# Performance work log

Hardware: AMD Instinct MI355X
Metric: run time of the kernel (lower is better)

## Reference

```python
import jax, jax.numpy as jnp
import numpy as np

# db1 (Haar) filters, replicating the torch module's pywt-derived constants.
_s = np.float32(1.0 / np.sqrt(2.0))
_dl = np.array([_s, _s], np.float32)    # dec_lo[::-1]
_dh = np.array([_s, -_s], np.float32)   # dec_hi[::-1]
_rl = np.array([_s, _s], np.float32)    # rec_lo
_rh = np.array([_s, -_s], np.float32)   # rec_hi
# filters[k][i,j] = a[j]*b[i]  (torch: a.unsqueeze(0)*b.unsqueeze(1)) == outer(b, a)
DEC = jnp.asarray(np.stack([np.outer(_dl, _dl) / 2.0, np.outer(_dh, _dl), np.outer(_dl, _dh), np.outer(_dh, _dh)], 0))  # [4,2,2]
REC = jnp.asarray(np.stack([np.outer(_rl, _rl) * 2.0, np.outer(_rh, _rl), np.outer(_rl, _rh), np.outer(_rh, _rh)], 0))  # [4,2,2]


def wt(x):
    # stride-2 2x2 conv per channel == linear mix of 2x2 blocks; fused over all channels
    B, C, H, W = x.shape
    xb = x.reshape(B, C, H // 2, 2, W // 2, 2)
    y = jnp.einsum('kpq,bchpwq->bckhw', DEC, xb)  # [B,C,4,H/2,W/2]
    y = jnp.concatenate([y[:, :, :1], (y[:, :, 1:] + 1.0) * 0.5], axis=2)  # rescale HF bands
    return y.reshape(B, 4 * C, H // 2, W // 2)


def iwt(y):
    B, C4, H, W = y.shape
    C = C4 // 4
    yb = y.reshape(B, C, 4, H, W)
    yb = jnp.concatenate([yb[:, :, :1], 2.0 * yb[:, :, 1:] - 1.0], axis=2)  # undo HF rescale
    x = jnp.einsum('kpq,bckhw->bchpwq', REC, yb)  # conv_transpose2d, stride 2, no overlap
    return x.reshape(B, C, 2 * H, 2 * W)


def conv3x3(x, w, b):
    y = jax.lax.conv_general_dilated(x, w, (1, 1), ((1, 1), (1, 1)), dimension_numbers=('NCHW', 'OIHW', 'NCHW'))
    return y + b[None, :, None, None]


def setup_inputs() -> dict:
    key = jax.random.key(0)
    ks = jax.random.split(key, 20)
    B, Cin, H, W = 8, 1, 512, 512
    c = 16
    inp = {'x': jax.random.normal(ks[0], (B, Cin, H, W), jnp.float32)}
    specs = [('conv1', c, 4 * Cin), ('conv2', 4 * c, 4 * c), ('conv3', 16 * c, 16 * c), ('conv4', 64 * c, 64 * c),
             ('convd1', 4, c), ('convd2', c, 2 * c), ('convd3', 4 * c, 8 * c), ('convd4', 16 * c, 32 * c)]
    for idx, (name, o, i) in enumerate(specs):
        kw, kb = jax.random.split(ks[1 + idx])
        inp[name + '_w'] = jax.random.normal(kw, (o, i, 3, 3), jnp.float32) / np.float32(np.sqrt(i * 9))
        inp[name + '_b'] = jax.random.normal(kb, (o,), jnp.float32) * 0.01
    return inp


def reference(x, conv1_w, conv1_b, conv2_w, conv2_b, conv3_w, conv3_b, conv4_w, conv4_b,
              convd1_w, convd1_b, convd2_w, convd2_b, convd3_w, convd3_b, convd4_w, convd4_b):
    lrelu = lambda t: jax.nn.leaky_relu(t, 0.2)
    w1 = wt(x);  c1 = lrelu(conv3x3(w1, conv1_w, conv1_b))
    w2 = wt(c1); c2 = lrelu(conv3x3(w2, conv2_w, conv2_b))
    w3 = wt(c2); c3 = lrelu(conv3x3(w3, conv3_w, conv3_b))
    w4 = wt(c3); c4 = lrelu(conv3x3(w4, conv4_w, conv4_b))
    c5 = lrelu(conv3x3(c4, conv4_w, conv4_b))  # conv4 reused, as in the torch module
    c6 = conv3x3(c5, conv4_w, conv4_b)
    ic4 = lrelu(c6 + w4)
    ic3 = lrelu(conv3x3(jnp.concatenate([c3, iwt(ic4)], 1), convd4_w, convd4_b))
    ic2 = lrelu(conv3x3(jnp.concatenate([c2, iwt(ic3)], 1), convd3_w, convd3_b))
    ic1 = lrelu(conv3x3(jnp.concatenate([c1, iwt(ic2)], 1), convd2_w, convd2_b))
    iw1 = lrelu(conv3x3(ic1, convd1_w, convd1_b))
    logits = iwt(iw1)
    return jax.nn.sigmoid(logits)
```

## Files before the change

kernel.cpp:

```cpp
#include <hip/hip_runtime.h>
#include <cstddef>


typedef unsigned short u16;
typedef unsigned int u32;
typedef __bf16 bf16x8 __attribute__((ext_vector_type(8)));
typedef float floatx4 __attribute__((ext_vector_type(4)));
typedef u16 u16x4 __attribute__((ext_vector_type(4)));
typedef u16 u16x8 __attribute__((ext_vector_type(8)));

__device__ __forceinline__ float b2f(u16 h) {
    union { u32 u; float f; } x; x.u = ((u32)h) << 16; return x.f;
}
__device__ __forceinline__ u16 f2b(float f) {
    union { float f; u32 u; } x; x.f = f;
    return (u16)((x.u + 0x7FFFu + ((x.u >> 16) & 1u)) >> 16);
}
__device__ __forceinline__ float lrelu_f(float v) { return v > 0.f ? v : 0.2f * v; }

__device__ __forceinline__ void gld16(const u16* g, u16* l) {
    __builtin_amdgcn_global_load_lds(
        (const __attribute__((address_space(1))) u32*)(const void*)g,
        (__attribute__((address_space(3))) u32*)(void*)l, 16, 0, 0);
}

template<int NT>
__global__ __launch_bounds__(256)
void conv_mfma_k(const u16* __restrict__ in, int Cin, int iWp, int iImg,
                 const u16* __restrict__ wb, const float* __restrict__ bias,
                 const u16* __restrict__ skip, int sC, int sWp, int sImg, int spad,
                 u16* __restrict__ out, int Cst, int oWp, int oImg, int opad,
                 int logW, int logH)
{
    constexpr int BM = 128, BN = NT * 32;
    constexpr int ASZ = BM * 32;
    constexpr int BSZ = BN * 32;
    __shared__ u16 At[2 * ASZ];
    __shared__ u16 Bt[2 * BSZ];

    const int tid = threadIdx.x;
    const int wid = tid >> 6, lane = tid & 63;
    const int W = 1 << logW, H = 1 << logH;
    const int mBase = blockIdx.x * BM;
    const int nBase = blockIdx.y * BN;
    const int K = 9 * Cin;
    const int kg = lane & 3;
    const int rr = lane >> 2;
    const int kgs = kg ^ ((rr >> 1) & 3);

    const u16 *gA0, *gA1, *gB0, *gB1 = nullptr;
    {
        int m0 = mBase + wid * 32 + rr;
        int px0 = m0 & (W - 1), py0 = (m0 >> logW) & (H - 1), pb0 = m0 >> (logW + logH);
        gA0 = in + ((size_t)pb0 * iImg + (size_t)py0 * iWp + px0) * Cin + kgs * 8;
        int m1 = m0 + 16;
        int px1 = m1 & (W - 1), py1 = (m1 >> logW) & (H - 1), pb1 = m1 >> (logW + logH);
        gA1 = in + ((size_t)pb1 * iImg + (size_t)py1 * iWp + px1) * Cin + kgs * 8;
    }
    if constexpr (NT == 4) {
        gB0 = wb + (size_t)(nBase + wid * 32 + rr) * K + kgs * 8;
        gB1 = wb + (size_t)(nBase + wid * 32 + 16 + rr) * K + kgs * 8;
    } else {
        gB0 = wb + (size_t)(nBase + wid * 16 + rr) * K + kgs * 8;
    }
    u16* lA0 = &At[wid * 1024];
    u16* lA1 = &At[wid * 1024 + 512];
    u16* lB0 = (NT == 4) ? &Bt[wid * 1024] : &Bt[wid * 512];
    u16* lB1 = (NT == 4) ? &Bt[wid * 1024 + 512] : nullptr;

    const int wm = wid >> 1, wn = wid & 1;
    const int fm = lane & 15;
    const int fk = ((lane >> 4) * 8) ^ (((fm >> 1) & 3) << 3);

    floatx4 acc[4][NT] = {};

    const int nChunks = K / 32;
    const size_t rowStep = (size_t)(iWp - 2) * Cin;
    int cbn = 0, tap = 0;

    auto stage = [&](int buf) {
        gld16(gA0, lA0 + buf * ASZ);
        gld16(gA1, lA1 + buf * ASZ);
        gld16(gB0, lB0 + buf * BSZ);
        if constexpr (NT == 4) gld16(gB1, lB1 + buf * BSZ);
        size_t dA = 32;
        cbn += 32;
        if (cbn == Cin) { cbn = 0; ++tap; dA = ((tap % 3 == 0) ? rowStep : (size_t)Cin) - (size_t)(Cin - 32); }
        gA0 += dA; gA1 += dA;
        gB0 += 32;
        if constexpr (NT == 4) gB1 += 32;
    };

    auto compute = [&](int buf) {
        const u16* Ab = &At[buf * ASZ];
        const u16* Bb = &Bt[buf * BSZ];
        bf16x8 af[4], bfr[NT];
#pragma unroll
        for (int mt = 0; mt < 4; ++mt)
            af[mt] = *(const bf16x8*)&Ab[(wm * 64 + mt * 16 + fm) * 32 + fk];
#pragma unroll
        for (int nt = 0; nt < NT; ++nt)
            bfr[nt] = *(const bf16x8*)&Bb[(wn * (NT * 16) + nt * 16 + fm) * 32 + fk];
        __builtin_amdgcn_s_setprio(1);
#pragma unroll
        for (int mt = 0; mt < 4; ++mt)
#pragma unroll
            for (int nt = 0; nt < NT; ++nt)
                acc[mt][nt] = __builtin_amdgcn_mfma_f32_16x16x32_bf16(af[mt], bfr[nt], acc[mt][nt], 0, 0, 0);
        __builtin_amdgcn_s_setprio(0);
    };

    stage(0);
    __syncthreads();
    for (int kc = 0; kc < nChunks; kc += 2) {
        stage(1);
        compute(0);
        __syncthreads();
        if (kc + 2 < nChunks) stage(0);
        compute(1);
        __syncthreads();
    }

    const int rq = (lane >> 4) * 4;
#pragma unroll
    for (int mt = 0; mt < 4; ++mt) {
        const int mrow = mBase + wm * 64 + mt * 16 + rq;
#pragma unroll
        for (int r = 0; r < 4; ++r) {
            int m2 = mrow + r;
            int px = m2 & (W - 1), py = (m2 >> logW) & (H - 1), pb = m2 >> (logW + logH);
            size_t ob = ((size_t)pb * oImg + (size_t)(py + opad) * oWp + (px + opad)) * Cst;
            size_t sb = 0;
            if (skip) sb = ((size_t)pb * sImg + (size_t)(py + spad) * sWp + (px + spad)) * sC;
#pragma unroll
            for (int nt = 0; nt < NT; ++nt) {
                int n = nBase + wn * (NT * 16) + nt * 16 + fm;
                float v = acc[mt][nt][r] + bias[n];
                if (skip) v += b2f(skip[sb + n]);
                v = lrelu_f(v);
                out[ob + n] = f2b(v);
            }
        }
    }
}

__global__ __launch_bounds__(256)
void conv_n16_k(const u16* __restrict__ in, int iWp, int iImg,
                const u16* __restrict__ wb, const float* __restrict__ bias,
                u16* __restrict__ out, int logW, int logH)
{
    __shared__ u16 At[128 * 32];
    __shared__ u16 Bt[16 * 32];
    const int tid = threadIdx.x;
    const int wid = tid >> 6, lane = tid & 63;
    const int W = 1 << logW, H = 1 << logH;
    const int mBase = blockIdx.x * 128;
    const int kg = lane & 3, rr = lane >> 2;
    const int kgs = kg ^ ((rr >> 1) & 3);

    const u16 *gA0, *gA1;
    {
        int m0 = mBase + wid * 32 + rr;
        int px0 = m0 & (W - 1), py0 = (m0 >> logW) & (H - 1), pb0 = m0 >> (logW + logH);
        gA0 = in + ((size_t)pb0 * iImg + (size_t)py0 * iWp + px0) * 32 + kgs * 8;
        int m1 = m0 + 16;
        int px1 = m1 & (W - 1), py1 = (m1 >> logW) & (H - 1), pb1 = m1 >> (logW + logH);
        gA1 = in + ((size_t)pb1 * iImg + (size_t)py1 * iWp + px1) * 32 + kgs * 8;
    }
    const u16* gB = wb + (size_t)rr * 288 + kgs * 8;
    u16* lA0 = &At[wid * 1024];
    u16* lA1 = &At[wid * 1024 + 512];

    const int fm = lane & 15;
    const int fk = ((lane >> 4) * 8) ^ (((fm >> 1) & 3) << 3);
    floatx4 acc[2] = {};
    const size_t rowStep = (size_t)(iWp - 2) * 32;

    for (int tap = 0; tap < 9; ++tap) {
        gld16(gA0, lA0);
        gld16(gA1, lA1);
        if (wid == 0) gld16(gB, &Bt[0]);
        __syncthreads();
        bf16x8 bf = *(const bf16x8*)&Bt[fm * 32 + fk];
#pragma unroll
        for (int mt = 0; mt < 2; ++mt) {
            bf16x8 af = *(const bf16x8*)&At[(wid * 32 + mt * 16 + fm) * 32 + fk];
            acc[mt] = __builtin_amdgcn_mfma_f32_16x16x32_bf16(af, bf, acc[mt], 0, 0, 0);
        }
        __syncthreads();
        size_t dA = (tap % 3 == 2) ? rowStep : (size_t)32;
        gA0 += dA; gA1 += dA; gB += 32;
    }

    const int rq = (lane >> 4) * 4;
    const float bn = bias[fm];
#pragma unroll
    for (int mt = 0; mt < 2; ++mt) {
#pragma unroll
        for (int r = 0; r < 4; ++r) {
            int m2 = mBase + wid * 32 + mt * 16 + rq + r;
            out[(size_t)m2 * 16 + fm] = f2b(lrelu_f(acc[mt][r] + bn));
        }
    }
}

template<int CIN, int COUT>
__global__ __launch_bounds__(256)
void conv_direct_k(const u16* __restrict__ in, int Sin,
                   const float* __restrict__ w, const float* __restrict__ bias,
                   u16* __restrict__ out, int Sout, int oWp, int oImg, int opad,
                   int logW, int logH, int total)
{
    int m = blockIdx.x * 256 + threadIdx.x;
    if (m >= total) return;
    const int W = 1 << logW, H = 1 << logH;
    const int px = m & (W - 1);
    const int py = (m >> logW) & (H - 1);
    const int pb = m >> (logW + logH);
    float acc[COUT];
#pragma unroll
    for (int o = 0; o < COUT; ++o) acc[o] = bias[o];
    for (int tap = 0; tap < 9; ++tap) {
        int dy = tap / 3 - 1, dx = tap % 3 - 1;
        int iy = py + dy, ix = px + dx;
        if ((unsigned)iy >= (unsigned)H || (unsigned)ix >= (unsigned)W) continue;
        const u16* p = in + (size_t)((((pb << logH) + iy) << logW) + ix) * Sin;
        if constexpr (CIN == 4) {
            u16x4 v = *(const u16x4*)p;
#pragma unroll
            for (int ci = 0; ci < 4; ++ci) {
                float f = b2f(v[ci]);
#pragma unroll
                for (int o = 0; o < COUT; ++o) acc[o] += f * w[(o * CIN + ci) * 9 + tap];
            }
        } else {
#pragma unroll
            for (int c8 = 0; c8 < CIN / 8; ++c8) {
                u16x8 v = *(const u16x8*)(p + c8 * 8);
#pragma unroll
                for (int j = 0; j < 8; ++j) {
                    int ci = c8 * 8 + j;
                    float f = b2f(v[j]);
#pragma unroll
                    for (int o = 0; o < COUT; ++o) acc[o] += f * w[(o * CIN + ci) * 9 + tap];
                }
            }
        }
    }
    size_t ob = ((size_t)pb * oImg + (size_t)(py + opad) * oWp + (px + opad)) * Sout;
#pragma unroll
    for (int o = 0; o < COUT; ++o)
        out[ob + o] = f2b(lrelu_f(acc[o]));
}

__global__ __launch_bounds__(256)
void wt_in_k(const float* __restrict__ x, u16* __restrict__ out, int total)
{
    int idx = blockIdx.x * 256 + threadIdx.x;
    if (idx >= total) return;
    int wq = idx & 255, t = idx >> 8;
    int hq = t & 255, b = t >> 8;
    const float* p = x + ((size_t)b * 512 + 2 * hq) * 512 + 2 * wq;
    float a = p[0], bv = p[1], cv = p[512], d = p[513];
    u16x4 o = { f2b(0.25f * (a + bv + cv + d)),
                f2b(0.25f * (a + bv - cv - d) + 0.5f),
                f2b(0.25f * (a - bv + cv - d) + 0.5f),
                f2b(0.25f * (a - bv - cv + d) + 0.5f) };
    *(u16x4*)&out[(size_t)idx * 4] = o;
}

__global__ __launch_bounds__(256)
void wt_k(const u16* __restrict__ in, int Sin, int iWp, int iImg, int ipad,
          u16* __restrict__ out, int Sout, int oWp, int oImg, int opad,
          int logC, int logWo, int logHo, int total)
{
    int idx = blockIdx.x * 256 + threadIdx.x;
    if (idx >= total) return;
    const int C = 1 << logC, Wo = 1 << logWo, Ho = 1 << logHo;
    int c = idx & (C - 1); int t = idx >> logC;
    int wq = t & (Wo - 1); t >>= logWo;
    int hq = t & (Ho - 1); int b = t >> logHo;
    size_t p00 = ((size_t)b * iImg + (size_t)(2 * hq + ipad) * iWp + (2 * wq + ipad)) * Sin + c;
    float a  = b2f(in[p00]);
    float bv = b2f(in[p00 + Sin]);
    float cv = b2f(in[p00 + (size_t)iWp * Sin]);
    float d  = b2f(in[p00 + (size_t)iWp * Sin + Sin]);
    u16x4 o = { f2b(0.25f * (a + bv + cv + d)),
                f2b(0.25f * (a + bv - cv - d) + 0.5f),
                f2b(0.25f * (a - bv + cv - d) + 0.5f),
                f2b(0.25f * (a - bv - cv + d) + 0.5f) };
    *(u16x4*)&out[((size_t)b * oImg + (size_t)(hq + opad) * oWp + (wq + opad)) * Sout + 4 * c] = o;
}

__global__ __launch_bounds__(256)
void iwt_k(const u16* __restrict__ in, int Sin, int logC, int logW, int logH,
           u16* __restrict__ out, int Sout, int oWp, int oImg, int opad, int total)
{
    int idx = blockIdx.x * 256 + threadIdx.x;
    if (idx >= total) return;
    const int C = 1 << logC, W = 1 << logW;
    int c = idx & (C - 1); int t = idx >> logC;
    int wq = t & (W - 1); t >>= logW;
    int hq = t & ((1 << logH) - 1); int b = t >> logH;
    u16x4 v = *(const u16x4*)&in[(size_t)((((b << logH) + hq) << logW) + wq) * Sin + 4 * c];
    float y0 = b2f(v[0]);
    float y1 = 2.f * b2f(v[1]) - 1.f;
    float y2 = 2.f * b2f(v[2]) - 1.f;
    float y3 = 2.f * b2f(v[3]) - 1.f;
    float x00 = y0 + 0.5f * ( y1 + y2 + y3);
    float x01 = y0 + 0.5f * ( y1 - y2 - y3);
    float x10 = y0 + 0.5f * (-y1 + y2 - y3);
    float x11 = y0 + 0.5f * (-y1 - y2 + y3);
    size_t q = ((size_t)b * oImg + (size_t)(2 * hq + opad) * oWp + (2 * wq + opad)) * Sout + c;
    out[q] = f2b(x00);
    out[q + Sout] = f2b(x01);
    out[q + (size_t)oWp * Sout] = f2b(x10);
    out[q + (size_t)oWp * Sout + Sout] = f2b(x11);
}

__global__ __launch_bounds__(256)
void iwt_out_k(const u16* __restrict__ in, float* __restrict__ out, int total)
{
    int idx = blockIdx.x * 256 + threadIdx.x;
    if (idx >= total) return;
    int wq = idx & 255, t = idx >> 8;
    int hq = t & 255, b = t >> 8;
    u16x4 v = *(const u16x4*)&in[(size_t)idx * 4];
    float y0 = b2f(v[0]);
    float y1 = 2.f * b2f(v[1]) - 1.f;
    float y2 = 2.f * b2f(v[2]) - 1.f;
    float y3 = 2.f * b2f(v[3]) - 1.f;
    float x00 = y0 + 0.5f * ( y1 + y2 + y3);
    float x01 = y0 + 0.5f * ( y1 - y2 - y3);
    float x10 = y0 + 0.5f * (-y1 + y2 - y3);
    float x11 = y0 + 0.5f * (-y1 - y2 + y3);
    float* q = out + ((size_t)b * 512 + 2 * hq) * 512 + 2 * wq;
    q[0]   = 1.f / (1.f + __expf(-x00));
    q[1]   = 1.f / (1.f + __expf(-x01));
    q[512] = 1.f / (1.f + __expf(-x10));
    q[513] = 1.f / (1.f + __expf(-x11));
}

__global__ __launch_bounds__(256)
void prep_w_k(const float* __restrict__ src, u16* __restrict__ dst, int logCIN, int total)
{
    int idx = blockIdx.x * 256 + threadIdx.x;
    if (idx >= total) return;
    const int CIN = 1 << logCIN;
    int ci = idx & (CIN - 1);
    int q = idx >> logCIN;
    int tap = q % 9, o = q / 9;
    dst[idx] = f2b(src[((size_t)(o * CIN + ci)) * 9 + tap]);
}

__global__ __launch_bounds__(256)
void zb_k(u16* __restrict__ buf, int Wp, int Hp, int C, int total)
{
    int idx = blockIdx.x * 256 + threadIdx.x;
    if (idx >= total) return;
    int c8 = idx % (C / 8); int t = idx / (C / 8);
    int nbp = 2 * Wp + 2 * (Hp - 2);
    int p = t % nbp; int b = t / nbp;
    int y, x;
    if (p < Wp) { y = 0; x = p; }
    else if (p < 2 * Wp) { y = Hp - 1; x = p - Wp; }
    else { int q = p - 2 * Wp; y = 1 + (q >> 1); x = (q & 1) ? Wp - 1 : 0; }
    u16x8 z = {0, 0, 0, 0, 0, 0, 0, 0};
    *(u16x8*)&buf[((size_t)b * Hp * Wp + (size_t)y * Wp + x) * C + c8 * 8] = z;
}

extern "C" void kernel_launch(void* const* d_in, const int* in_sizes, int n_in,
                              void* d_out, int out_size, void* d_ws, size_t ws_size,
                              hipStream_t stream)
{
    const float* x   = (const float*)d_in[0];
    const float* c1w = (const float*)d_in[1];  const float* c1b = (const float*)d_in[2];
    const float* c2w = (const float*)d_in[3];  const float* c2b = (const float*)d_in[4];
    const float* c3w = (const float*)d_in[5];  const float* c3b = (const float*)d_in[6];
    const float* c4w = (const float*)d_in[7];  const float* c4b = (const float*)d_in[8];
    const float* d1w = (const float*)d_in[9];  const float* d1b = (const float*)d_in[10];
    const float* d2w = (const float*)d_in[11]; const float* d2b = (const float*)d_in[12];
    const float* d3w = (const float*)d_in[13]; const float* d3b = (const float*)d_in[14];
    const float* d4w = (const float*)d_in[15]; const float* d4b = (const float*)d_in[16];

    const size_t MiB = 1u << 20;
    char* base = (char*)d_ws;
    u16* c4wb = (u16*)base;
    u16* c3wb = c4wb + 9437184;
    u16* d4wb = c3wb + 589824;
    u16* d3wb = d4wb + 1179648;
    u16* c2wb = d3wb + 73728;
    u16* d2wb = c2wb + 36864;
    u16* CAT1p = (u16*)(base + 22  * MiB);
    u16* CAT2p = (u16*)(base + 55  * MiB);
    u16* CAT3p = (u16*)(base + 88  * MiB);
    u16* P1    = (u16*)(base + 123 * MiB);
    u16* P2    = (u16*)(base + 142 * MiB);
    u16* P3    = (u16*)(base + 161 * MiB);
    float* outp = (float*)d_out;

    u16* W2p = P1; u16* W4p = P1; u16* IC2 = P1;
    u16* W3p = P2; u16* C4p = P2; u16* IC4 = P2; u16* IC1 = P2;
    u16* W1  = P3; u16* C5p = P3; u16* IC3 = P3; u16* IW1 = P3;

    auto cdiv = [](int a, int b) { return (a + b - 1) / b; };
    auto prep = [&](const float* s, u16* d, int logCIN, int total) {
        prep_w_k<<<cdiv(total, 256), 256, 0, stream>>>(s, d, logCIN, total);
    };
    auto zb = [&](u16* buf, int Wp, int Hp, int C) {
        int total = 8 * (2 * Wp + 2 * (Hp - 2)) * (C / 8);
        zb_k<<<cdiv(total, 256), 256, 0, stream>>>(buf, Wp, Hp, C, total);
    };
    auto mfma = [&](const u16* in, int Cin, int iWp, int iImg,
                    const u16* w, const float* bi,
                    const u16* skip, int sC, int sWp, int sImg, int spad,
                    int Cout, u16* out, int Cst, int oWp, int oImg, int opad,
                    int logW, int logH) {
        int M = 8 << (logW + logH);
        if (Cout % 128 == 0) {
            dim3 g(M / 128, Cout / 128);
            conv_mfma_k<4><<<g, 256, 0, stream>>>(in, Cin, iWp, iImg, w, bi,
                                                  skip, sC, sWp, sImg, spad,
                                                  out, Cst, oWp, oImg, opad, logW, logH);
        } else {
            dim3 g(M / 128, Cout / 64);
            conv_mfma_k<2><<<g, 256, 0, stream>>>(in, Cin, iWp, iImg, w, bi,
                                                  skip, sC, sWp, sImg, spad,
                                                  out, Cst, oWp, oImg, opad, logW, logH);
        }
    };

    prep(c4w, c4wb, 10, 9437184);
    prep(c3w, c3wb, 8, 589824);
    prep(d4w, d4wb, 9, 1179648);
    prep(d3w, d3wb, 7, 73728);
    prep(c2w, c2wb, 6, 36864);
    prep(d2w, d2wb, 5, 4608);
    zb(CAT1p, 258, 258, 32);
    zb(W2p, 130, 130, 64);
    zb(W3p, 66, 66, 256);
    zb(CAT2p, 130, 130, 128);
    zb(CAT3p, 66, 66, 512);

    const int P256 = 8 * 256 * 256;
    const int T2M = 2097152;
    const int I258 = 258 * 258;

    wt_in_k<<<cdiv(P256, 256), 256, 0, stream>>>(x, W1, P256);
    conv_direct_k<4, 16><<<cdiv(P256, 256), 256, 0, stream>>>(
        W1, 4, c1w, c1b, CAT1p, 32, 258, I258, 1, 8, 8, P256);
    zb(C5p, 34, 34, 1024);
    wt_k<<<cdiv(T2M, 256), 256, 0, stream>>>(CAT1p, 32, 258, I258, 1,
                                             W2p, 64, 130, 16900, 1, 4, 7, 7, T2M);
    mfma(W2p, 64, 130, 16900, c2wb, c2b, nullptr, 0, 0, 0, 0,
         64, CAT2p, 128, 130, 16900, 1, 7, 7);
    zb(W4p, 34, 34, 1024);
    wt_k<<<cdiv(T2M, 256), 256, 0, stream>>>(CAT2p, 128, 130, 16900, 1,
                                             W3p, 256, 66, 4356, 1, 6, 6, 6, T2M);
    mfma(W3p, 256, 66, 4356, c3wb, c3b, nullptr, 0, 0, 0, 0,
         256, CAT3p, 512, 66, 4356, 1, 6, 6);
    zb(C4p, 34, 34, 1024);
    wt_k<<<cdiv(T2M, 256), 256, 0, stream>>>(CAT3p, 512, 66, 4356, 1,
                                             W4p, 1024, 34, 1156, 1, 8, 5, 5, T2M);
    mfma(W4p, 1024, 34, 1156, c4wb, c4b, nullptr, 0, 0, 0, 0,
         1024, C4p, 1024, 34, 1156, 1, 5, 5);
    mfma(C4p, 1024, 34, 1156, c4wb, c4b, nullptr, 0, 0, 0, 0,
         1024, C5p, 1024, 34, 1156, 1, 5, 5);
    mfma(C5p, 1024, 34, 1156, c4wb, c4b, W4p, 1024, 34, 1156, 1,
         1024, IC4, 1024, 32, 1024, 0, 5, 5);
    iwt_k<<<cdiv(T2M, 256), 256, 0, stream>>>(IC4, 1024, 8, 5, 5,
                                              CAT3p + 256, 512, 66, 4356, 1, T2M);
    mfma(CAT3p, 512, 66, 4356, d4wb, d4b, nullptr, 0, 0, 0, 0,
         256, IC3, 256, 64, 4096, 0, 6, 6);
    iwt_k<<<cdiv(T2M, 256), 256, 0, stream>>>(IC3, 256, 6, 6, 6,
                                              CAT2p + 64, 128, 130, 16900, 1, T2M);
    mfma(CAT2p, 128, 130, 16900, d3wb, d3b, nullptr, 0, 0, 0, 0,
         64, IC2, 64, 128, 16384, 0, 7, 7);
    iwt_k<<<cdiv(T2M, 256), 256, 0, stream>>>(IC2, 64, 4, 7, 7,
                                              CAT1p + 16, 32, 258, I258, 1, T2M);
    conv_n16_k<<<dim3(P256 / 128), 256, 0, stream>>>(CAT1p, 258, I258, d2wb, d2b, IC1, 8, 8);
    conv_direct_k<16, 4><<<cdiv(P256, 256), 256, 0, stream>>>(
        IC1, 16, d1w, d1b, IW1, 4, 256, 65536, 0, 8, 8, P256);
    iwt_out_k<<<cdiv(P256, 256), 256, 0, stream>>>(IW1, outp, P256);
}
```

Baseline: 1.034 ms.

## Deepen NT=4 conv pipeline to multi-buffered LDS with explicit vmcnt waits

For the NT=4 MFMA conv kernel, the A tiles are now held in 4 LDS buffers and the B tiles in 6. The main loop is unrolled over 12-chunk macro-iterations that prefetch two chunks ahead. The old __syncthreads is replaced with an s_waitcnt vmcnt(4) plus barrier, so only the oldest loads must land before compute continues. Launch bounds now ask for 2 blocks per CU. The goal is to hide global-load latency better, at the cost of more LDS per block, which may limit occupancy. The schedule also assumes nChunks is a multiple of 12 and at least 12.

```diff
diff --git a/kernel.cpp b/kernel.cpp
--- a/kernel.cpp
+++ b/kernel.cpp
@@ -24,8 +24,11 @@
         (__attribute__((address_space(3))) u32*)(void*)l, 16, 0, 0);
 }
 
+#define WB4 asm volatile("s_waitcnt vmcnt(4) lgkmcnt(0)\ns_barrier" ::: "memory")
+#define WB0 asm volatile("s_waitcnt vmcnt(0) lgkmcnt(0)\ns_barrier" ::: "memory")
+
 template<int NT>
-__global__ __launch_bounds__(256)
+__global__ __launch_bounds__(256, 2)
 void conv_mfma_k(const u16* __restrict__ in, int Cin, int iWp, int iImg,
                  const u16* __restrict__ wb, const float* __restrict__ bias,
                  const u16* __restrict__ skip, int sC, int sWp, int sImg, int spad,
@@ -35,8 +38,10 @@
     constexpr int BM = 128, BN = NT * 32;
     constexpr int ASZ = BM * 32;
     constexpr int BSZ = BN * 32;
-    __shared__ u16 At[2 * ASZ];
-    __shared__ u16 Bt[2 * BSZ];
+    constexpr int ANB = (NT == 4) ? 4 : 2;
+    constexpr int BNB = (NT == 4) ? 6 : 2;
+    __shared__ u16 At[ANB * ASZ];
+    __shared__ u16 Bt[BNB * BSZ];
 
     const int tid = threadIdx.x;
     const int wid = tid >> 6, lane = tid & 63;
@@ -78,22 +83,25 @@
     const size_t rowStep = (size_t)(iWp - 2) * Cin;
     int cbn = 0, tap = 0;
 
-    auto stage = [&](int buf) {
+    auto stageA = [&](int buf) {
         gld16(gA0, lA0 + buf * ASZ);
         gld16(gA1, lA1 + buf * ASZ);
-        gld16(gB0, lB0 + buf * BSZ);
-        if constexpr (NT == 4) gld16(gB1, lB1 + buf * BSZ);
         size_t dA = 32;
         cbn += 32;
         if (cbn == Cin) { cbn = 0; ++tap; dA = ((tap % 3 == 0) ? rowStep : (size_t)Cin) - (size_t)(Cin - 32); }
         gA0 += dA; gA1 += dA;
+    };
+
+    auto stageB = [&](int buf) {
+        gld16(gB0, lB0 + buf * BSZ);
+        if constexpr (NT == 4) gld16(gB1, lB1 + buf * BSZ);
         gB0 += 32;
         if constexpr (NT == 4) gB1 += 32;
     };
 
-    auto compute = [&](int buf) {
-        const u16* Ab = &At[buf * ASZ];
-        const u16* Bb = &Bt[buf * BSZ];
+    auto compute = [&](int ab, int bb) {
+        const u16* Ab = &At[ab * ASZ];
+        const u16* Bb = &Bt[bb * BSZ];
         bf16x8 af[4], bfr[NT];
 #pragma unroll
         for (int mt = 0; mt < 4; ++mt)
@@ -110,15 +118,36 @@
         __builtin_amdgcn_s_setprio(0);
     };
 
-    stage(0);
-    __syncthreads();
-    for (int kc = 0; kc < nChunks; kc += 2) {
-        stage(1);
-        compute(0);
+    if constexpr (NT == 4) {
+        stageA(0); stageA(1);
+        stageB(0); stageB(1); stageB(2); stageB(3);
+        WB4;
+        const int nMac = nChunks / 12;
+        for (int it = 0; it < nMac - 1; ++it) {
+            stageA(2); stageA(3); stageB(4); stageB(5); compute(0, 0); compute(1, 1); WB4;
+            stageA(0); stageA(1); stageB(0); stageB(1); compute(2, 2); compute(3, 3); WB4;
+            stageA(2); stageA(3); stageB(2); stageB(3); compute(0, 4); compute(1, 5); WB4;
+            stageA(0); stageA(1); stageB(4); stageB(5); compute(2, 0); compute(3, 1); WB4;
+            stageA(2); stageA(3); stageB(0); stageB(1); compute(0, 2); compute(1, 3); WB4;
+            stageA(0); stageA(1); stageB(2); stageB(3); compute(2, 4); compute(3, 5); WB4;
+        }
+        stageA(2); stageA(3); stageB(4); stageB(5); compute(0, 0); compute(1, 1); WB4;
+        stageA(0); stageA(1); stageB(0); stageB(1); compute(2, 2); compute(3, 3); WB4;
+        stageA(2); stageA(3); stageB(2); stageB(3); compute(0, 4); compute(1, 5); WB4;
+        stageA(0); stageA(1); stageB(4); stageB(5); compute(2, 0); compute(3, 1); WB4;
+        stageA(2); stageA(3);                       compute(0, 2); compute(1, 3); WB0;
+        compute(2, 4); compute(3, 5);
+    } else {
+        stageA(0); stageB(0);
         __syncthreads();
-        if (kc + 2 < nChunks) stage(0);
-        compute(1);
-        __syncthreads();
+        for (int kc = 0; kc < nChunks; kc += 2) {
+            stageA(1); stageB(1);
+            compute(0, 0);
+            __syncthreads();
+            if (kc + 2 < nChunks) { stageA(0); stageB(0); }
+            compute(1, 1);
+            __syncthreads();
+        }
     }
 
     const int rq = (lane >> 4) * 4;
@@ -128,10 +157,10 @@
 #pragma unroll
         for (int r = 0; r < 4; ++r) {
             int m2 = mrow + r;
-            int px = m2 & (W - 1), py = (m2 >> logW) & (H - 1), pb = m2 >> (logW + logH);
-            size_t ob = ((size_t)pb * oImg + (size_t)(py + opad) * oWp + (px + opad)) * Cst;
+            int px = m2 & (W - 1), py = (m2 >> logW) & (H - 1), pb2 = m2 >> (logW + logH);
+            size_t ob = ((size_t)pb2 * oImg + (size_t)(py + opad) * oWp + (px + opad)) * Cst;
             size_t sb = 0;
-            if (skip) sb = ((size_t)pb * sImg + (size_t)(py + spad) * sWp + (px + spad)) * sC;
+            if (skip) sb = ((size_t)pb2 * sImg + (size_t)(py + spad) * sWp + (px + spad)) * sC;
 #pragma unroll
             for (int nt = 0; nt < NT; ++nt) {
                 int n = nBase + wn * (NT * 16) + nt * 16 + fm;
```

Result: faster. 907.3 us (-12.3%).
